# Performance work log

Measured on AMD Instinct MI355X. Metric: run time of the kernel, lower is better.

The kernel has to match this reference:

```python
import jax, jax.numpy as jnp
import numpy as np

C = 37       # number of tidal constituents (AstroCache.num_constituents)
B = 65536    # batch size
W = 30       # layer_width


def _mlp(x, W1, b1, W2, b2, W3, b3, Wo, bo):
    """Batched ConstituentWeightBlock over C constituents.
    Structure per torch Sequential: Linear(2,W) -> Linear(W,W)+ReLU -> Linear(W,W)+ReLU -> Linear(W,1).
    Note: no ReLU after the first linear.
    x: [B,2]; W1: [C,W,2]; W2,W3: [C,W,W]; Wo: [C,W]. Returns [C,B]."""
    h = jnp.einsum('bd,cod->cbo', x, W1) + b1[:, None, :]                 # [C,B,W]
    h = jax.nn.relu(jnp.einsum('cbi,coi->cbo', h, W2) + b2[:, None, :])   # [C,B,W]
    h = jax.nn.relu(jnp.einsum('cbi,coi->cbo', h, W3) + b3[:, None, :])   # [C,B,W]
    return jnp.einsum('cbi,ci->cb', h, Wo) + bo[:, None]                  # [C,B]


def setup_inputs() -> dict:
    key = jax.random.key(0)
    ks = iter(jax.random.split(key, 32))
    s = 0.1  # weight init scale
    inp = {
        'x': jax.random.normal(next(ks), (B, 2), jnp.float32),
        'a': jax.random.normal(next(ks), (C, B), jnp.float32) * 0.5,
        'u': jax.random.normal(next(ks), (C, B), jnp.float32),
        'f': jax.random.uniform(next(ks), (C, B), jnp.float32),
        'V': jax.random.normal(next(ks), (C, B), jnp.float32),
        't_hours_offset': jax.random.uniform(next(ks), (B,), jnp.float32) * 24.0,
        'bias': jnp.zeros((1,), jnp.float32),
    }
    for pre in ('H', 'P'):
        inp[f'W{pre}1'] = jax.random.normal(next(ks), (C, W, 2), jnp.float32) * s
        inp[f'b{pre}1'] = jax.random.normal(next(ks), (C, W), jnp.float32) * s
        inp[f'W{pre}2'] = jax.random.normal(next(ks), (C, W, W), jnp.float32) * s
        inp[f'b{pre}2'] = jax.random.normal(next(ks), (C, W), jnp.float32) * s
        inp[f'W{pre}3'] = jax.random.normal(next(ks), (C, W, W), jnp.float32) * s
        inp[f'b{pre}3'] = jax.random.normal(next(ks), (C, W), jnp.float32) * s
        inp[f'W{pre}o'] = jax.random.normal(next(ks), (C, W), jnp.float32) * s
        inp[f'b{pre}o'] = jax.random.normal(next(ks), (C,), jnp.float32) * s
    return inp


def reference(x, a, u, f, V, t_hours_offset, bias,
              WH1, bH1, WH2, bH2, WH3, bH3, WHo, bHo,
              WP1, bP1, WP2, bP2, WP3, bP3, WPo, bPo):
    H = _mlp(x, WH1, bH1, WH2, bH2, WH3, bH3, WHo, bHo)   # amplitude weights [C,B]
    p = _mlp(x, WP1, bP1, WP2, bP2, WP3, bP3, WPo, bPo)   # phase offsets    [C,B]
    phase = V + a * t_hours_offset[None, :] + u - p        # [C,B]
    height = bias[0] + jnp.sum(H * f * jnp.cos(phase), axis=0)  # [B]
    return height[:, None]                                  # [B,1]
```

## Files before the change

### kernel.cpp

```cpp
#include <hip/hip_runtime.h>
#include <math.h>

#define NC 37
#define NW 30

#define REPEAT30(M) M(0) M(1) M(2) M(3) M(4) M(5) M(6) M(7) M(8) M(9) \
                    M(10) M(11) M(12) M(13) M(14) M(15) M(16) M(17) M(18) M(19) \
                    M(20) M(21) M(22) M(23) M(24) M(25) M(26) M(27) M(28) M(29)
#define REPEAT30P(M,o) M(o,0) M(o,1) M(o,2) M(o,3) M(o,4) M(o,5) M(o,6) M(o,7) \
                       M(o,8) M(o,9) M(o,10) M(o,11) M(o,12) M(o,13) M(o,14) M(o,15) \
                       M(o,16) M(o,17) M(o,18) M(o,19) M(o,20) M(o,21) M(o,22) M(o,23) \
                       M(o,24) M(o,25) M(o,26) M(o,27) M(o,28) M(o,29)

__global__ __launch_bounds__(256) void tide_init(float* __restrict__ out,
                                                 const float* __restrict__ bias,
                                                 int n) {
    int i = blockIdx.x * 256 + threadIdx.x;
    if (i < n) out[i] = bias[0];
}

__device__ __forceinline__ float mlp_eval(
    float x0, float x1,
    const float* __restrict__ w1, const float* __restrict__ b1,
    const float* __restrict__ w2, const float* __restrict__ b2,
    const float* __restrict__ w3, const float* __restrict__ b3,
    const float* __restrict__ wo, float bo)
{
#define DECLH(i) float h##i;
    REPEAT30(DECLH)
#define DECLG(i) float g##i;
    REPEAT30(DECLG)

#define LAYER1(i) h##i = fmaf(w1[2*(i)], x0, fmaf(w1[2*(i)+1], x1, b1[(i)]));
    REPEAT30(LAYER1)

#define FMA2(o,i) acc = fmaf(w2[(o)*NW+(i)], h##i, acc);
#define LAYER2(o) { float acc = b2[(o)]; REPEAT30P(FMA2,o) g##o = fmaxf(acc, 0.0f); }
    REPEAT30(LAYER2)

#define FMA3(o,i) acc = fmaf(w3[(o)*NW+(i)], g##i, acc);
#define LAYER3(o) { float acc = b3[(o)]; REPEAT30P(FMA3,o) h##o = fmaxf(acc, 0.0f); }
    REPEAT30(LAYER3)

    float r = bo;
#define OUTL(i) r = fmaf(wo[(i)], h##i, r);
    REPEAT30(OUTL)
    return r;

#undef DECLH
#undef DECLG
#undef LAYER1
#undef FMA2
#undef LAYER2
#undef FMA3
#undef LAYER3
#undef OUTL
}

__global__ __launch_bounds__(256, 3) void tide_main(
    const float* __restrict__ x, const float* __restrict__ a,
    const float* __restrict__ u, const float* __restrict__ f,
    const float* __restrict__ V, const float* __restrict__ t,
    const float* __restrict__ WH1, const float* __restrict__ bH1,
    const float* __restrict__ WH2, const float* __restrict__ bH2,
    const float* __restrict__ WH3, const float* __restrict__ bH3,
    const float* __restrict__ WHo, const float* __restrict__ bHo,
    const float* __restrict__ WP1, const float* __restrict__ bP1,
    const float* __restrict__ WP2, const float* __restrict__ bP2,
    const float* __restrict__ WP3, const float* __restrict__ bP3,
    const float* __restrict__ WPo, const float* __restrict__ bPo,
    float* __restrict__ out, int B)
{
    const int c = blockIdx.y;
    const int b = blockIdx.x * 256 + threadIdx.x;
    if (b >= B) return;

    const float x0 = x[2*b];
    const float x1 = x[2*b + 1];

    const float Hv = mlp_eval(x0, x1,
                              WH1 + c*NW*2, bH1 + c*NW,
                              WH2 + c*NW*NW, bH2 + c*NW,
                              WH3 + c*NW*NW, bH3 + c*NW,
                              WHo + c*NW, bHo[c]);
    const float pv = mlp_eval(x0, x1,
                              WP1 + c*NW*2, bP1 + c*NW,
                              WP2 + c*NW*NW, bP2 + c*NW,
                              WP3 + c*NW*NW, bP3 + c*NW,
                              WPo + c*NW, bPo[c]);

    const long cb = (long)c * B + b;
    const float phase = V[cb] + a[cb] * t[b] + u[cb] - pv;
    atomicAdd(&out[b], Hv * f[cb] * cosf(phase));
}

extern "C" void kernel_launch(void* const* d_in, const int* in_sizes, int n_in,
                              void* d_out, int out_size, void* d_ws, size_t ws_size,
                              hipStream_t stream) {
    const float* x    = (const float*)d_in[0];
    const float* a    = (const float*)d_in[1];
    const float* u    = (const float*)d_in[2];
    const float* f    = (const float*)d_in[3];
    const float* V    = (const float*)d_in[4];
    const float* t    = (const float*)d_in[5];
    const float* bias = (const float*)d_in[6];
    const float* WH1  = (const float*)d_in[7];
    const float* bH1  = (const float*)d_in[8];
    const float* WH2  = (const float*)d_in[9];
    const float* bH2  = (const float*)d_in[10];
    const float* WH3  = (const float*)d_in[11];
    const float* bH3  = (const float*)d_in[12];
    const float* WHo  = (const float*)d_in[13];
    const float* bHo  = (const float*)d_in[14];
    const float* WP1  = (const float*)d_in[15];
    const float* bP1  = (const float*)d_in[16];
    const float* WP2  = (const float*)d_in[17];
    const float* bP2  = (const float*)d_in[18];
    const float* WP3  = (const float*)d_in[19];
    const float* bP3  = (const float*)d_in[20];
    const float* WPo  = (const float*)d_in[21];
    const float* bPo  = (const float*)d_in[22];
    float* out = (float*)d_out;

    const int B = in_sizes[0] / 2;

    tide_init<<<(out_size + 255) / 256, 256, 0, stream>>>(out, bias, out_size);

    dim3 grid((B + 255) / 256, NC);
    tide_main<<<grid, 256, 0, stream>>>(x, a, u, f, V, t,
                                        WH1, bH1, WH2, bH2, WH3, bH3, WHo, bHo,
                                        WP1, bP1, WP2, bP2, WP3, bP3, WPo, bPo,
                                        out, B);
}
```

Before: 692.0 us.

## Load MLP weights via explicit scalar loads and replace atomics with workspace reduction

Weight rows are now fetched with inline-asm s_load_dwordx8/x4/x2 into SGPRs, one row at a time followed by a waitcnt. Each row is accumulated with two interleaved FMA chains to shorten the dependency chain. When the workspace is large enough, per-constituent contributions are written to it and summed by a separate reduce kernel instead of using global atomicAdd. The explicit waitcnt per row serialises the scalar loads with the math, and the workspace path adds extra memory traffic plus one more launch.

```diff
diff --git a/kernel.cpp b/kernel.cpp
--- a/kernel.cpp
+++ b/kernel.cpp
@@ -3,14 +3,92 @@
 
 #define NC 37
 #define NW 30
+
+typedef __attribute__((ext_vector_type(8))) unsigned int su8;
+typedef __attribute__((ext_vector_type(4))) unsigned int su4;
+typedef __attribute__((ext_vector_type(2))) unsigned int su2;
+
+#define uf(x) __uint_as_float(x)
+
+#define SLD8_0(d, p)   asm volatile("s_load_dwordx8 %0, %1, 0x0"  : "=s"(d) : "s"(p))
+#define SLD8_32(d, p)  asm volatile("s_load_dwordx8 %0, %1, 0x20" : "=s"(d) : "s"(p))
+#define SLD8_64(d, p)  asm volatile("s_load_dwordx8 %0, %1, 0x40" : "=s"(d) : "s"(p))
+#define SLD4_96(d, p)  asm volatile("s_load_dwordx4 %0, %1, 0x60" : "=s"(d) : "s"(p))
+#define SLD2_112(d, p) asm volatile("s_load_dwordx2 %0, %1, 0x70" : "=s"(d) : "s"(p))
+#define SLD2_0(d, p)   asm volatile("s_load_dwordx2 %0, %1, 0x0"  : "=s"(d) : "s"(p))
+#define SLD1_0(d, p)   asm volatile("s_load_dword %0, %1, 0x0"    : "=s"(d) : "s"(p))
 
 #define REPEAT30(M) M(0) M(1) M(2) M(3) M(4) M(5) M(6) M(7) M(8) M(9) \
                     M(10) M(11) M(12) M(13) M(14) M(15) M(16) M(17) M(18) M(19) \
                     M(20) M(21) M(22) M(23) M(24) M(25) M(26) M(27) M(28) M(29)
-#define REPEAT30P(M,o) M(o,0) M(o,1) M(o,2) M(o,3) M(o,4) M(o,5) M(o,6) M(o,7) \
-                       M(o,8) M(o,9) M(o,10) M(o,11) M(o,12) M(o,13) M(o,14) M(o,15) \
-                       M(o,16) M(o,17) M(o,18) M(o,19) M(o,20) M(o,21) M(o,22) M(o,23) \
-                       M(o,24) M(o,25) M(o,26) M(o,27) M(o,28) M(o,29)
+
+#define RELUF(v) fmaxf((v), 0.0f)
+#define IDF(v) (v)
+
+#define ROW30(SRC) \
+  acc0 = fmaf(uf(Aq[0]), SRC##0, acc0);  acc1 = fmaf(uf(Aq[1]), SRC##1, acc1); \
+  acc0 = fmaf(uf(Aq[2]), SRC##2, acc0);  acc1 = fmaf(uf(Aq[3]), SRC##3, acc1); \
+  acc0 = fmaf(uf(Aq[4]), SRC##4, acc0);  acc1 = fmaf(uf(Aq[5]), SRC##5, acc1); \
+  acc0 = fmaf(uf(Aq[6]), SRC##6, acc0);  acc1 = fmaf(uf(Aq[7]), SRC##7, acc1); \
+  acc0 = fmaf(uf(Bq[0]), SRC##8, acc0);  acc1 = fmaf(uf(Bq[1]), SRC##9, acc1); \
+  acc0 = fmaf(uf(Bq[2]), SRC##10, acc0); acc1 = fmaf(uf(Bq[3]), SRC##11, acc1); \
+  acc0 = fmaf(uf(Bq[4]), SRC##12, acc0); acc1 = fmaf(uf(Bq[5]), SRC##13, acc1); \
+  acc0 = fmaf(uf(Bq[6]), SRC##14, acc0); acc1 = fmaf(uf(Bq[7]), SRC##15, acc1); \
+  acc0 = fmaf(uf(Cq[0]), SRC##16, acc0); acc1 = fmaf(uf(Cq[1]), SRC##17, acc1); \
+  acc0 = fmaf(uf(Cq[2]), SRC##18, acc0); acc1 = fmaf(uf(Cq[3]), SRC##19, acc1); \
+  acc0 = fmaf(uf(Cq[4]), SRC##20, acc0); acc1 = fmaf(uf(Cq[5]), SRC##21, acc1); \
+  acc0 = fmaf(uf(Cq[6]), SRC##22, acc0); acc1 = fmaf(uf(Cq[7]), SRC##23, acc1); \
+  acc0 = fmaf(uf(Dq[0]), SRC##24, acc0); acc1 = fmaf(uf(Dq[1]), SRC##25, acc1); \
+  acc0 = fmaf(uf(Dq[2]), SRC##26, acc0); acc1 = fmaf(uf(Dq[3]), SRC##27, acc1); \
+  acc0 = fmaf(uf(Eq[0]), SRC##28, acc0); acc1 = fmaf(uf(Eq[1]), SRC##29, acc1);
+
+#define LROW(o, wp, bp, SRC, DST, APPLY) { \
+  su8 Aq, Bq, Cq; su4 Dq; su2 Eq; unsigned int bbv; \
+  const float* rp_ = (wp) + (o)*NW; const float* bp_ = (bp) + (o); \
+  SLD8_0(Aq, rp_); SLD8_32(Bq, rp_); SLD8_64(Cq, rp_); \
+  SLD4_96(Dq, rp_); SLD2_112(Eq, rp_); SLD1_0(bbv, bp_); \
+  asm volatile("s_waitcnt lgkmcnt(0)" \
+    : "+s"(Aq), "+s"(Bq), "+s"(Cq), "+s"(Dq), "+s"(Eq), "+s"(bbv)); \
+  float acc0 = uf(bbv), acc1 = 0.0f; \
+  ROW30(SRC) \
+  DST = APPLY(acc0 + acc1); }
+
+#define L1OUT(o, wp, bp, DST) { \
+  su2 Wv; unsigned int bbv; \
+  const float* rp_ = (wp) + 2*(o); const float* bp_ = (bp) + (o); \
+  SLD2_0(Wv, rp_); SLD1_0(bbv, bp_); \
+  asm volatile("s_waitcnt lgkmcnt(0)" : "+s"(Wv), "+s"(bbv)); \
+  DST = fmaf(uf(Wv[0]), x0v, fmaf(uf(Wv[1]), x1v, uf(bbv))); }
+
+__device__ __forceinline__ float mlp_eval(
+    float x0v, float x1v,
+    const float* __restrict__ w1, const float* __restrict__ b1,
+    const float* __restrict__ w2, const float* __restrict__ b2,
+    const float* __restrict__ w3, const float* __restrict__ b3,
+    const float* __restrict__ wo, const float* __restrict__ boP)
+{
+#define DECLH(i) float h##i;
+    REPEAT30(DECLH)
+#define DECLG(i) float g##i;
+    REPEAT30(DECLG)
+
+#define DO_L1(o) L1OUT(o, w1, b1, h##o)
+    REPEAT30(DO_L1)
+#define DO_L2(o) LROW(o, w2, b2, h, g##o, RELUF)
+    REPEAT30(DO_L2)
+#define DO_L3(o) LROW(o, w3, b3, g, h##o, RELUF)
+    REPEAT30(DO_L3)
+
+    float res;
+    LROW(0, wo, boP, h, res, IDF)
+    return res;
+
+#undef DECLH
+#undef DECLG
+#undef DO_L1
+#undef DO_L2
+#undef DO_L3
+}
 
 __global__ __launch_bounds__(256) void tide_init(float* __restrict__ out,
                                                  const float* __restrict__ bias,
@@ -19,44 +97,18 @@
     if (i < n) out[i] = bias[0];
 }
 
-__device__ __forceinline__ float mlp_eval(
-    float x0, float x1,
-    const float* __restrict__ w1, const float* __restrict__ b1,
-    const float* __restrict__ w2, const float* __restrict__ b2,
-    const float* __restrict__ w3, const float* __restrict__ b3,
-    const float* __restrict__ wo, float bo)
-{
-#define DECLH(i) float h##i;
-    REPEAT30(DECLH)
-#define DECLG(i) float g##i;
-    REPEAT30(DECLG)
-
-#define LAYER1(i) h##i = fmaf(w1[2*(i)], x0, fmaf(w1[2*(i)+1], x1, b1[(i)]));
-    REPEAT30(LAYER1)
-
-#define FMA2(o,i) acc = fmaf(w2[(o)*NW+(i)], h##i, acc);
-#define LAYER2(o) { float acc = b2[(o)]; REPEAT30P(FMA2,o) g##o = fmaxf(acc, 0.0f); }
-    REPEAT30(LAYER2)
-
-#define FMA3(o,i) acc = fmaf(w3[(o)*NW+(i)], g##i, acc);
-#define LAYER3(o) { float acc = b3[(o)]; REPEAT30P(FMA3,o) h##o = fmaxf(acc, 0.0f); }
-    REPEAT30(LAYER3)
-
-    float r = bo;
-#define OUTL(i) r = fmaf(wo[(i)], h##i, r);
-    REPEAT30(OUTL)
-    return r;
-
-#undef DECLH
-#undef DECLG
-#undef LAYER1
-#undef FMA2
-#undef LAYER2
-#undef FMA3
-#undef LAYER3
-#undef OUTL
-}
-
+__global__ __launch_bounds__(256) void tide_reduce(const float* __restrict__ ws,
+                                                   const float* __restrict__ bias,
+                                                   float* __restrict__ out, int B) {
+    int b = blockIdx.x * 256 + threadIdx.x;
+    if (b >= B) return;
+    float s = bias[0];
+    #pragma unroll
+    for (int c = 0; c < NC; ++c) s += ws[(long)c * B + b];
+    out[b] = s;
+}
+
+template<int MODE>
 __global__ __launch_bounds__(256, 3) void tide_main(
     const float* __restrict__ x, const float* __restrict__ a,
     const float* __restrict__ u, const float* __restrict__ f,
@@ -69,29 +121,35 @@
     const float* __restrict__ WP2, const float* __restrict__ bP2,
     const float* __restrict__ WP3, const float* __restrict__ bP3,
     const float* __restrict__ WPo, const float* __restrict__ bPo,
-    float* __restrict__ out, int B)
+    float* __restrict__ dst, int B)
 {
     const int c = blockIdx.y;
     const int b = blockIdx.x * 256 + threadIdx.x;
     if (b >= B) return;
 
-    const float x0 = x[2*b];
-    const float x1 = x[2*b + 1];
-
-    const float Hv = mlp_eval(x0, x1,
+    const float x0v = x[2*b];
+    const float x1v = x[2*b + 1];
+
+    const float Hv = mlp_eval(x0v, x1v,
                               WH1 + c*NW*2, bH1 + c*NW,
                               WH2 + c*NW*NW, bH2 + c*NW,
                               WH3 + c*NW*NW, bH3 + c*NW,
-                              WHo + c*NW, bHo[c]);
-    const float pv = mlp_eval(x0, x1,
+                              WHo + c*NW, bHo + c);
+    const float pv = mlp_eval(x0v, x1v,
                               WP1 + c*NW*2, bP1 + c*NW,
                               WP2 + c*NW*NW, bP2 + c*NW,
                               WP3 + c*NW*NW, bP3 + c*NW,
-                              WPo + c*NW, bPo[c]);
+                              WPo + c*NW, bPo + c);
 
     const long cb = (long)c * B + b;
     const float phase = V[cb] + a[cb] * t[b] + u[cb] - pv;
-    atomicAdd(&out[b], Hv * f[cb] * cosf(phase));
+    const float contrib = Hv * f[cb] * cosf(phase);
+
+    if (MODE == 0) {
+        dst[cb] = contrib;
+    } else {
+        atomicAdd(&dst[b], contrib);
+    }
 }
 
 extern "C" void kernel_launch(void* const* d_in, const int* in_sizes, int n_in,
@@ -123,12 +181,21 @@
     float* out = (float*)d_out;
 
     const int B = in_sizes[0] / 2;
-
-    tide_init<<<(out_size + 255) / 256, 256, 0, stream>>>(out, bias, out_size);
+    const size_t ws_needed = (size_t)NC * (size_t)B * sizeof(float);
 
     dim3 grid((B + 255) / 256, NC);
-    tide_main<<<grid, 256, 0, stream>>>(x, a, u, f, V, t,
-                                        WH1, bH1, WH2, bH2, WH3, bH3, WHo, bHo,
-                                        WP1, bP1, WP2, bP2, WP3, bP3, WPo, bPo,
-                                        out, B);
-}
+    if (ws_size >= ws_needed) {
+        float* ws = (float*)d_ws;
+        tide_main<0><<<grid, 256, 0, stream>>>(x, a, u, f, V, t,
+                                               WH1, bH1, WH2, bH2, WH3, bH3, WHo, bHo,
+                                               WP1, bP1, WP2, bP2, WP3, bP3, WPo, bPo,
+                                               ws, B);
+        tide_reduce<<<(B + 255) / 256, 256, 0, stream>>>(ws, bias, out, B);
+    } else {
+        tide_init<<<(out_size + 255) / 256, 256, 0, stream>>>(out, bias, out_size);
+        tide_main<1><<<grid, 256, 0, stream>>>(x, a, u, f, V, t,
+                                               WH1, bH1, WH2, bH2, WH3, bH3, WHo, bHo,
+                                               WP1, bP1, WP2, bP2, WP3, bP3, WPo, bPo,
+                                               out, B);
+    }
+}
```

Measured after the change: 842.0 us. +21.7%, slower.
